# Performance work log

Hardware: AMD Instinct MI355X
Metric: run time of the kernel (lower is better)

## Reference

```python
import jax, jax.numpy as jnp
import numpy as np
from jax import lax

N_NODES = 16384
N_EDGES = 262144
T = 64
F_IN = 8
H1, C1 = 12, 16          # globals H and O in the source
HID2 = H1 * C1           # 192, input to second GATConv
LSTM_H = 128
TRAIN_LEN = 32
TARGET_ID = 0
NEG_SLOPE = 0.2


def setup_inputs() -> dict:
    key = jax.random.key(0)
    ks = jax.random.split(key, 16)
    x = jax.random.normal(ks[0], (T, N_NODES, F_IN), jnp.float32)
    src = jax.random.randint(ks[1], (T, N_EDGES), 0, N_NODES)
    dst = jax.random.randint(ks[2], (T, N_EDGES), 0, N_NODES)
    dst = jnp.where(dst == src, (dst + 1) % N_NODES, dst)  # guarantee no self-loops
    edge_index = jnp.stack([src, dst], axis=1)  # (T, 2, E)
    g = lambda k, sh: jax.random.normal(k, sh, jnp.float32) * 0.1
    return {
        "x": x, "edge_index": edge_index,
        "Wl1": g(ks[3], (F_IN, H1 * C1)),
        "att_l1": g(ks[4], (1, H1, C1)), "att_r1": g(ks[5], (1, H1, C1)),
        "b1": jnp.zeros((H1 * C1,), jnp.float32),
        "Wl2": g(ks[6], (HID2, 1)),
        "att_l2": g(ks[7], (1, 1, 1)), "att_r2": g(ks[8], (1, 1, 1)),
        "b2": jnp.zeros((1,), jnp.float32),
        "Wih0": g(ks[9], (4 * LSTM_H, 1)), "Whh0": g(ks[10], (4 * LSTM_H, LSTM_H)),
        "bih0": jnp.zeros((4 * LSTM_H,), jnp.float32), "bhh0": jnp.zeros((4 * LSTM_H,), jnp.float32),
        "Wih1": g(ks[11], (4 * LSTM_H, LSTM_H)), "Whh1": g(ks[12], (4 * LSTM_H, LSTM_H)),
        "bih1": jnp.zeros((4 * LSTM_H,), jnp.float32), "bhh1": jnp.zeros((4 * LSTM_H,), jnp.float32),
        "Wlin": g(ks[13], (1, LSTM_H)), "blin": jnp.zeros((1,), jnp.float32),
    }


def _gat(x, ei, W, att_l, att_r, b, heads, outc, concat):
    N = x.shape[0]
    xl = (x @ W).reshape(N, heads, outc)              # (N,H,C)
    al = jnp.sum(xl * att_l, axis=-1)                 # (N,H)
    ar = jnp.sum(xl * att_r, axis=-1)                 # (N,H)
    loop = jnp.arange(N)
    src = jnp.concatenate([ei[0], loop])              # add self loops (inputs have none)
    dst = jnp.concatenate([ei[1], loop])
    alpha = jax.nn.leaky_relu(al[src] + ar[dst], NEG_SLOPE)  # (E+N, H)
    # segment softmax over destination neighborhoods
    amax = jax.ops.segment_max(alpha, dst, num_segments=N)
    ex = jnp.exp(alpha - amax[dst])
    alpha = ex / (jax.ops.segment_sum(ex, dst, num_segments=N)[dst] + 1e-16)
    # hardcoded per-edge-row edits from message(): s and v copies, then blend
    s = alpha.at[jnp.array([1, 2, 12, 19, 22])].set(0.0).at[jnp.array([7, 14])].set(1.0)
    v = alpha.at[jnp.array([10, 13])].set(0.5).at[jnp.array([17])].set(0.0)
    alpha = 0.8 * alpha + 0.1 * s + 0.1 * v
    out = jax.ops.segment_sum(xl[src] * alpha[:, :, None], dst, num_segments=N)  # (N,H,C)
    out = out.reshape(N, heads * outc) if concat else out.mean(axis=1)
    return out + b


def _lstm_layer(xs, Wih, Whh, bih, bhh):
    # xs: (L, B, in) -> hs: (L, B, H); torch gate order i,f,g,o
    Bsz, Hd = xs.shape[1], Whh.shape[1]
    def step(carry, xt):
        h, c = carry
        gates = xt @ Wih.T + h @ Whh.T + bih + bhh
        i, f, g, o = jnp.split(gates, 4, axis=-1)
        c = jax.nn.sigmoid(f) * c + jax.nn.sigmoid(i) * jnp.tanh(g)
        h = jax.nn.sigmoid(o) * jnp.tanh(c)
        return (h, c), h
    init = (jnp.zeros((Bsz, Hd), xs.dtype), jnp.zeros((Bsz, Hd), xs.dtype))
    _, hs = lax.scan(step, init, xs)
    return hs


def reference(x, edge_index, Wl1, att_l1, att_r1, b1, Wl2, att_l2, att_r2, b2,
              Wih0, Whh0, bih0, bhh0, Wih1, Whh1, bih1, bhh1, Wlin, blin):
    def per_t(args):
        xt, eit = args
        h = _gat(xt, eit, Wl1, att_l1, att_r1, b1, H1, C1, True)
        h = jax.nn.elu(h)
        h = _gat(h, eit, Wl2, att_l2, att_r2, b2, 1, 1, False)
        return h[:, 0]
    out = lax.map(per_t, (x, edge_index))             # (T, N) == xs_out
    series = lax.stop_gradient(out[:, TARGET_ID])     # split_sequences detaches
    idx = jnp.arange(T - TRAIN_LEN)[:, None] + jnp.arange(TRAIN_LEN)[None, :]
    ts = series[idx][:, :, None]                      # (B, L, 1), batch_first
    xs = jnp.transpose(ts, (1, 0, 2))                 # (L, B, 1)
    hs = _lstm_layer(xs, Wih0, Whh0, bih0, bhh0)
    hs = _lstm_layer(hs, Wih1, Whh1, bih1, bhh1)
    return hs[-1] @ Wlin.T + blin                     # (B, 1)
```

## Files before the change

kernel.cpp:

```cpp
#include <hip/hip_runtime.h>
#include <math.h>

#define T 64
#define NN 16384
#define NE 262144
#define FIN 8
#define H1H 12
#define C1C 16
#define HID 192
#define CAP2 95
#define SCAP 96
#define DEGCAP 127
#define LH 128
#define G4 512
#define NB 32
#define NL 32

#define DEV __device__ __forceinline__

DEV float wave_max(float v){
  #pragma unroll
  for (int m = 32; m; m >>= 1) v = fmaxf(v, __shfl_xor(v, m));
  return v;
}
DEV float wave_sum(float v){
  #pragma unroll
  for (int m = 32; m; m >>= 1) v += __shfl_xor(v, m);
  return v;
}
DEV float leaky(float x){ return x >= 0.f ? x : 0.2f * x; }
DEV float sigmoidf(float x){ return 1.f / (1.f + expf(-x)); }

DEV float apply_edit(float a, int eid){
  if (eid >= 32) return a;
  const unsigned m09 = (1u<<1)|(1u<<2)|(1u<<7)|(1u<<10)|(1u<<12)|(1u<<13)|(1u<<14)|(1u<<17)|(1u<<19)|(1u<<22);
  const unsigned mp1 = (1u<<7)|(1u<<14);
  const unsigned mp05 = (1u<<10)|(1u<<13);
  unsigned b = 1u << eid;
  float r = (m09 & b) ? 0.9f * a : a;
  if (mp1 & b) r += 0.1f;
  if (mp05 & b) r += 0.05f;
  return r;
}

__global__ __launch_bounds__(256) void k_scan0(const int* __restrict__ ei,
                                               int* __restrict__ cnt2, int* __restrict__ list2){
  long long gid = (long long)blockIdx.x * blockDim.x + threadIdx.x;
  long long e4 = gid * 4;
  int t = (int)(e4 >> 18);
  int e = (int)(e4 & (NE - 1));
  const int* dstp = ei + (size_t)t * 2 * NE + NE + e;
  int4 d = *(const int4*)dstp;
  int dd[4] = {d.x, d.y, d.z, d.w};
  #pragma unroll
  for (int q = 0; q < 4; q++){
    if (dd[q] == 0){
      int pos = atomicAdd(&cnt2[t], 1);
      if (pos < CAP2) list2[t * CAP2 + pos] = e + q;
    }
  }
}

__global__ __launch_bounds__(128) void k_build(const int* __restrict__ ei, const int* __restrict__ cnt2,
                                               const int* __restrict__ list2, int* __restrict__ scnt,
                                               int* __restrict__ Slist, int* __restrict__ slot_of){
  int t = blockIdx.x;
  int* so = slot_of + (size_t)t * NN;
  int m = min(cnt2[t], CAP2);
  for (int i = threadIdx.x; i < m + 1; i += blockDim.x){
    int u = (i == m) ? 0 : ei[(size_t)t * 2 * NE + list2[t * CAP2 + i]];
    int old = atomicCAS(&so[u], -1, -2);
    if (old == -1){
      int s = atomicAdd(&scnt[t], 1);
      Slist[t * SCAP + s] = u;
      __hip_atomic_store(&so[u], s, __ATOMIC_RELAXED, __HIP_MEMORY_SCOPE_AGENT);
    }
  }
}

__global__ __launch_bounds__(256) void k_scan1(const int* __restrict__ ei, const int* __restrict__ slot_of,
                                               int* __restrict__ ecnt1, int* __restrict__ elist1){
  long long gid = (long long)blockIdx.x * blockDim.x + threadIdx.x;
  long long e4 = gid * 4;
  int t = (int)(e4 >> 18);
  int e = (int)(e4 & (NE - 1));
  const int* dstp = ei + (size_t)t * 2 * NE + NE + e;
  int4 d = *(const int4*)dstp;
  int dd[4] = {d.x, d.y, d.z, d.w};
  #pragma unroll
  for (int q = 0; q < 4; q++){
    int sl = slot_of[(size_t)t * NN + dd[q]];
    if (sl >= 0){
      int pos = atomicAdd(&ecnt1[t * SCAP + sl], 1);
      if (pos < DEGCAP) elist1[((size_t)t * SCAP + sl) * DEGCAP + pos] = e + q;
    }
  }
}

__global__ __launch_bounds__(64, 4) void k_gat1(const float* __restrict__ x, const int* __restrict__ ei,
                                             const float* __restrict__ Wl1, const float* __restrict__ attl,
                                             const float* __restrict__ attr, const float* __restrict__ b1,
                                             const int* __restrict__ scnt, const int* __restrict__ Slist,
                                             const int* __restrict__ ecnt1, const int* __restrict__ elist1,
                                             float* __restrict__ h1){
  int t = blockIdx.y, s = blockIdx.x, h = blockIdx.z;
  if (s >= scnt[t]) return;
  int lane = threadIdx.x;
  int u = Slist[t * SCAP + s];
  int deg = min(ecnt1[t * SCAP + s], DEGCAP);
  int tot = deg + 1;
  bool two = tot > 64;
  const float* xt = x + (size_t)t * NN * FIN;
  const int* srcp = ei + (size_t)t * 2 * NE;
  const int* el = elist1 + ((size_t)t * SCAP + s) * DEGCAP;

  float4 xu_a = ((const float4*)(xt + (size_t)u * FIN))[0];
  float4 xu_b = ((const float4*)(xt + (size_t)u * FIN))[1];
  float xu[FIN] = {xu_a.x, xu_a.y, xu_a.z, xu_a.w, xu_b.x, xu_b.y, xu_b.z, xu_b.w};

  bool act0 = lane < tot;
  int eid0 = 1 << 29;
  int su0 = u;
  if (lane < deg){ int e = el[lane]; eid0 = e; su0 = srcp[e]; }
  float4 xs0a = ((const float4*)(xt + (size_t)su0 * FIN))[0];
  float4 xs0b = ((const float4*)(xt + (size_t)su0 * FIN))[1];
  float xsrc0[FIN] = {xs0a.x, xs0a.y, xs0a.z, xs0a.w, xs0b.x, xs0b.y, xs0b.z, xs0b.w};

  bool act1 = false; int eid1 = 1 << 29;
  float xsrc1[FIN];
  if (two){
    int idx = 64 + lane;
    act1 = idx < tot;
    int su1 = u;
    if (idx < deg){ int e = el[idx]; eid1 = e; su1 = srcp[e]; }
    float4 xs1a = ((const float4*)(xt + (size_t)su1 * FIN))[0];
    float4 xs1b = ((const float4*)(xt + (size_t)su1 * FIN))[1];
    #pragma unroll
    for (int f = 0; f < 4; f++) xsrc1[f] = (&xs1a.x)[f];
    #pragma unroll
    for (int f = 0; f < 4; f++) xsrc1[4 + f] = (&xs1b.x)[f];
  }

  const float* Wh = Wl1 + h * C1C;
  const float* attlh = attl + h * C1C;
  const float* attrh = attr + h * C1C;

  float ar = 0.f;
  #pragma unroll
  for (int c = 0; c < C1C; c++){
    float v = 0.f;
    #pragma unroll
    for (int f = 0; f < FIN; f++) v = fmaf(xu[f], Wh[f * HID + c], v);
    ar = fmaf(v, attrh[c], ar);
  }

  float xls0[C1C];
  float al0 = 0.f;
  #pragma unroll
  for (int c = 0; c < C1C; c++){
    float v = 0.f;
    #pragma unroll
    for (int f = 0; f < FIN; f++) v = fmaf(xsrc0[f], Wh[f * HID + c], v);
    xls0[c] = v;
    al0 = fmaf(v, attlh[c], al0);
  }
  float raw0 = act0 ? leaky(al0 + ar) : -INFINITY;

  float xls1[C1C];
  float raw1 = -INFINITY;
  if (two){
    float al1 = 0.f;
    #pragma unroll
    for (int c = 0; c < C1C; c++){
      float v = 0.f;
      #pragma unroll
      for (int f = 0; f < FIN; f++) v = fmaf(xsrc1[f], Wh[f * HID + c], v);
      xls1[c] = v;
      al1 = fmaf(v, attlh[c], al1);
    }
    raw1 = act1 ? leaky(al1 + ar) : -INFINITY;
  }

  float M = wave_max(fmaxf(raw0, raw1));
  float ex0 = act0 ? expf(raw0 - M) : 0.f;
  float ex1 = act1 ? expf(raw1 - M) : 0.f;
  float S = wave_sum(ex0 + ex1);
  float den = S + 1e-16f;
  float alpha0 = apply_edit(ex0 / den, eid0);
  float alpha1 = two ? apply_edit(ex1 / den, eid1) : 0.f;

  float sum[C1C];
  #pragma unroll
  for (int c = 0; c < C1C; c++){
    sum[c] = xls0[c] * alpha0;
    if (two) sum[c] = fmaf(xls1[c], alpha1, sum[c]);
  }
  #pragma unroll
  for (int m = 32; m; m >>= 1){
    #pragma unroll
    for (int c = 0; c < C1C; c++) sum[c] += __shfl_xor(sum[c], m);
  }
  if (lane == 0){
    float* h1p = h1 + ((size_t)t * SCAP + s) * HID + h * C1C;
    #pragma unroll
    for (int c = 0; c < C1C; c++){
      float v = sum[c] + b1[h * C1C + c];
      h1p[c] = v > 0.f ? v : expm1f(v);
    }
  }
}

__global__ __launch_bounds__(64) void k_gat2(const int* __restrict__ ei, const float* __restrict__ Wl2,
                                             const float* __restrict__ attl2_, const float* __restrict__ attr2_,
                                             const float* __restrict__ b2, const int* __restrict__ cnt2,
                                             const int* __restrict__ list2, const int* __restrict__ slot_of,
                                             const float* __restrict__ h1, float* __restrict__ series){
  int t = blockIdx.x; int lane = threadIdx.x;
  int deg = min(cnt2[t], CAP2);
  int tot = deg + 1;
  const int* srcp = ei + (size_t)t * 2 * NE;
  const int* so = slot_of + (size_t)t * NN;
  float attl2 = attl2_[0], attr2 = attr2_[0];
  int sl0 = so[0];
  const float* h1t = h1 + (size_t)t * SCAP * HID;

  float x0 = 0.f;
  for (int k = 0; k < HID; k++) x0 += h1t[(size_t)sl0 * HID + k] * Wl2[k];

  bool act[2]; int eid[2]; float xl2[2];
  #pragma unroll
  for (int ch = 0; ch < 2; ch++){
    int idx = ch * 64 + lane;
    act[ch] = idx < tot;
    eid[ch] = 1 << 29;
    int sl = sl0;
    if (idx < deg){ int e = list2[t * CAP2 + idx]; eid[ch] = e; sl = so[srcp[e]]; }
    float v = 0.f;
    if (act[ch]) for (int k = 0; k < HID; k++) v += h1t[(size_t)sl * HID + k] * Wl2[k];
    xl2[ch] = v;
  }
  float raw[2];
  #pragma unroll
  for (int ch = 0; ch < 2; ch++) raw[ch] = act[ch] ? leaky(attl2 * xl2[ch] + attr2 * x0) : -INFINITY;
  float M = wave_max(fmaxf(raw[0], raw[1]));
  float ex[2];
  #pragma unroll
  for (int ch = 0; ch < 2; ch++) ex[ch] = act[ch] ? expf(raw[ch] - M) : 0.f;
  float S = wave_sum(ex[0] + ex[1]);
  float den = S + 1e-16f;
  float contrib = apply_edit(ex[0] / den, eid[0]) * xl2[0] + apply_edit(ex[1] / den, eid[1]) * xl2[1];
  contrib = wave_sum(contrib);
  if (lane == 0) series[t] = contrib + b2[0];
}

#define AT_LOADR(p)    __hip_atomic_load((p), __ATOMIC_RELAXED, __HIP_MEMORY_SCOPE_AGENT)
#define AT_STORER(p,v) __hip_atomic_store((p), (v), __ATOMIC_RELAXED, __HIP_MEMORY_SCOPE_AGENT)

#define REP32(M) M(0)M(1)M(2)M(3)M(4)M(5)M(6)M(7)M(8)M(9)M(10)M(11)M(12)M(13)M(14)M(15)\
                 M(16)M(17)M(18)M(19)M(20)M(21)M(22)M(23)M(24)M(25)M(26)M(27)M(28)M(29)M(30)M(31)
#define WDECL(i) float4 w##i;
#define WLOAD(i) w##i = Wr[i];
#define WPIN(i)  asm volatile("" : "+v"(w##i.x), "+v"(w##i.y), "+v"(w##i.z), "+v"(w##i.w));
#define WFMA(i)  { float4 hv = h4[i]; a0 = fmaf(w##i.x, hv.x, a0); a1 = fmaf(w##i.y, hv.y, a1); \
                   a2 = fmaf(w##i.z, hv.z, a2); a3 = fmaf(w##i.w, hv.w, a3); }

__global__ __launch_bounds__(512, 2) void k_lstm(const float* __restrict__ series,
    const float* __restrict__ Wih0, const float* __restrict__ Whh0,
    const float* __restrict__ bih0, const float* __restrict__ bhh0,
    const float* __restrict__ Wih1, const float* __restrict__ Whh1,
    const float* __restrict__ bih1, const float* __restrict__ bhh1,
    const float* __restrict__ Wlin, const float* __restrict__ blin,
    float* __restrict__ h0g, float* __restrict__ xpart,
    int* __restrict__ flagA, int* __restrict__ flagB, float* __restrict__ out){
  int j = threadIdx.x;
  int st = blockIdx.x >> 5;
  int b = blockIdx.x & 31;
  __shared__ __align__(16) float h_lds[LH];
  __shared__ __align__(16) float c_lds[LH];
  __shared__ float gate_lds[G4];
  __shared__ float s_series[NL];
  __shared__ int rdy_lds;
  const float4* h4 = (const float4*)h_lds;

  if (st == 0){
    const float4* Wr = (const float4*)(Whh0 + (size_t)j * LH);
    REP32(WDECL)
    REP32(WLOAD)
    REP32(WPIN)
    float wih = Wih0[j];
    float bsum = bih0[j] + bhh0[j];
    if (j < LH){ h_lds[j] = 0.f; c_lds[j] = 0.f; }
    if (j < NL) s_series[j] = series[b + j];
    __syncthreads();
    for (int t = 0; t < NL; t++){
      float a0 = 0.f, a1 = 0.f, a2 = 0.f, a3 = 0.f;
      REP32(WFMA)
      float acc = fmaf(wih, s_series[t], bsum) + (a0 + a1) + (a2 + a3);
      gate_lds[j] = acc;
      __syncthreads();
      if (j < LH){
        float ig = sigmoidf(gate_lds[j]);
        float fg = sigmoidf(gate_lds[LH + j]);
        float gg = tanhf(gate_lds[2 * LH + j]);
        float og = sigmoidf(gate_lds[3 * LH + j]);
        float c = fg * c_lds[j] + ig * gg;
        float h = og * tanhf(c);
        c_lds[j] = c; h_lds[j] = h;
        AT_STORER(&h0g[(b * NL + t) * LH + j], h);
      }
      __syncthreads();
      if (j == 0) AT_STORER(&flagA[b], t + 1);
    }
  } else if (st == 1){
    const float4* Wr = (const float4*)(Wih1 + (size_t)j * LH);
    REP32(WDECL)
    REP32(WLOAD)
    REP32(WPIN)
    int ready = 0;
    for (int t = 0; t < NL; t++){
      if (ready <= t){
        if (j == 0){
          int f;
          while ((f = AT_LOADR(&flagA[b])) < t + 1) __builtin_amdgcn_s_sleep(1);
          rdy_lds = f;
        }
        __syncthreads();
        ready = rdy_lds;
      }
      if (j < LH) h_lds[j] = AT_LOADR(&h0g[(b * NL + t) * LH + j]);
      __syncthreads();
      float a0 = 0.f, a1 = 0.f, a2 = 0.f, a3 = 0.f;
      REP32(WFMA)
      AT_STORER(&xpart[(b * NL + t) * G4 + j], (a0 + a1) + (a2 + a3));
      __syncthreads();
      if (j == 0) AT_STORER(&flagB[b], t + 1);
    }
  } else {
    const float4* Wr = (const float4*)(Whh1 + (size_t)j * LH);
    REP32(WDECL)
    REP32(WLOAD)
    REP32(WPIN)
    float bsum = bih1[j] + bhh1[j];
    if (j < LH){ h_lds[j] = 0.f; c_lds[j] = 0.f; }
    __syncthreads();
    int ready = 0;
    for (int t = 0; t < NL; t++){
      if (ready <= t){
        if (j == 0){
          int f;
          while ((f = AT_LOADR(&flagB[b])) < t + 1) __builtin_amdgcn_s_sleep(1);
          rdy_lds = f;
        }
        __syncthreads();
        ready = rdy_lds;
      }
      float xj = AT_LOADR(&xpart[(b * NL + t) * G4 + j]);
      float a0 = 0.f, a1 = 0.f, a2 = 0.f, a3 = 0.f;
      REP32(WFMA)
      float acc = xj + bsum + (a0 + a1) + (a2 + a3);
      gate_lds[j] = acc;
      __syncthreads();
      if (j < LH){
        float ig = sigmoidf(gate_lds[j]);
        float fg = sigmoidf(gate_lds[LH + j]);
        float gg = tanhf(gate_lds[2 * LH + j]);
        float og = sigmoidf(gate_lds[3 * LH + j]);
        float c = fg * c_lds[j] + ig * gg;
        float h = og * tanhf(c);
        c_lds[j] = c; h_lds[j] = h;
      }
      __syncthreads();
    }
    if (j == 0){
      float s2 = blin[0];
      for (int k = 0; k < LH; k++) s2 += Wlin[k] * h_lds[k];
      out[b] = s2;
    }
  }
}

extern "C" void kernel_launch(void* const* d_in, const int* in_sizes, int n_in,
                              void* d_out, int out_size, void* d_ws, size_t ws_size,
                              hipStream_t stream) {
  const float* x     = (const float*)d_in[0];
  const int*   ei    = (const int*)  d_in[1];
  const float* Wl1   = (const float*)d_in[2];
  const float* attl1 = (const float*)d_in[3];
  const float* attr1 = (const float*)d_in[4];
  const float* b1    = (const float*)d_in[5];
  const float* Wl2   = (const float*)d_in[6];
  const float* attl2 = (const float*)d_in[7];
  const float* attr2 = (const float*)d_in[8];
  const float* b2    = (const float*)d_in[9];
  const float* Wih0  = (const float*)d_in[10];
  const float* Whh0  = (const float*)d_in[11];
  const float* bih0  = (const float*)d_in[12];
  const float* bhh0  = (const float*)d_in[13];
  const float* Wih1  = (const float*)d_in[14];
  const float* Whh1  = (const float*)d_in[15];
  const float* bih1  = (const float*)d_in[16];
  const float* bhh1  = (const float*)d_in[17];
  const float* Wlin  = (const float*)d_in[18];
  const float* blin  = (const float*)d_in[19];
  float* out = (float*)d_out;

  char* wsb = (char*)d_ws;
  size_t off = 0;
  auto alloc = [&](size_t bytes)->void*{
    void* p = wsb + off;
    off += (bytes + 255) & ~(size_t)255;
    return p;
  };
  int* cnt2  = (int*)alloc(T * 4);
  int* scnt  = (int*)alloc(T * 4);
  int* ecnt1 = (int*)alloc(T * SCAP * 4);
  int* flagA = (int*)alloc(NB * 4);
  int* flagB = (int*)alloc(NB * 4);
  size_t ctrl_bytes = off;
  int* slot_of = (int*)alloc((size_t)T * NN * 4);
  int* list2   = (int*)alloc((size_t)T * CAP2 * 4);
  int* Slist   = (int*)alloc((size_t)T * SCAP * 4);
  int* elist1  = (int*)alloc((size_t)T * SCAP * DEGCAP * 4);
  float* h1    = (float*)alloc((size_t)T * SCAP * HID * 4);
  float* series= (float*)alloc(T * 4);
  float* h0g   = (float*)alloc((size_t)NB * NL * LH * 4);
  float* xpart = (float*)alloc((size_t)NB * NL * G4 * 4);

  hipMemsetAsync(d_ws, 0, ctrl_bytes, stream);
  hipMemsetAsync(slot_of, 0xFF, (size_t)T * NN * 4, stream);

  k_scan0<<<T * NE / 4 / 256, 256, 0, stream>>>(ei, cnt2, list2);
  k_build<<<T, 128, 0, stream>>>(ei, cnt2, list2, scnt, Slist, slot_of);
  k_scan1<<<T * NE / 4 / 256, 256, 0, stream>>>(ei, slot_of, ecnt1, elist1);
  k_gat1<<<dim3(SCAP, T, H1H), 64, 0, stream>>>(x, ei, Wl1, attl1, attr1, b1, scnt, Slist, ecnt1, elist1, h1);
  k_gat2<<<T, 64, 0, stream>>>(ei, Wl2, attl2, attr2, b2, cnt2, list2, slot_of, h1, series);
  k_lstm<<<96, 512, 0, stream>>>(series, Wih0, Whh0, bih0, bhh0, Wih1, Whh1, bih1, bhh1,
                                 Wlin, blin, h0g, xpart, flagA, flagB, out);
}
```

Measured before the change: 415.7 us.

## Compact GAT1 work list and split LSTM weights between registers and LDS

k_build now appends each (t, slot) pair to a global work list. k_gat1 runs as a persistent grid-stride kernel over that list times the heads, instead of a sparse 3D grid where most blocks exit early. In the LSTM kernel only half of each weight row stays pinned in registers and the other half is staged transposed in LDS, which cuts register pressure at the cost of LDS reads every step. The LSTM consumer waits now poll the flag every step instead of caching a readiness counter.

```diff
diff --git a/kernel.cpp b/kernel.cpp
--- a/kernel.cpp
+++ b/kernel.cpp
@@ -63,7 +63,8 @@
 
 __global__ __launch_bounds__(128) void k_build(const int* __restrict__ ei, const int* __restrict__ cnt2,
                                                const int* __restrict__ list2, int* __restrict__ scnt,
-                                               int* __restrict__ Slist, int* __restrict__ slot_of){
+                                               int* __restrict__ Slist, int* __restrict__ slot_of,
+                                               int* __restrict__ wcnt, int* __restrict__ wlist){
   int t = blockIdx.x;
   int* so = slot_of + (size_t)t * NN;
   int m = min(cnt2[t], CAP2);
@@ -73,6 +74,8 @@
     if (old == -1){
       int s = atomicAdd(&scnt[t], 1);
       Slist[t * SCAP + s] = u;
+      int w = atomicAdd(wcnt, 1);
+      wlist[w] = (t << 8) | s;
       __hip_atomic_store(&so[u], s, __ATOMIC_RELAXED, __HIP_MEMORY_SCOPE_AGENT);
     }
   }
@@ -97,115 +100,125 @@
   }
 }
 
-__global__ __launch_bounds__(64, 4) void k_gat1(const float* __restrict__ x, const int* __restrict__ ei,
+__global__ __launch_bounds__(256, 4) void k_gat1(const float* __restrict__ x, const int* __restrict__ ei,
                                              const float* __restrict__ Wl1, const float* __restrict__ attl,
                                              const float* __restrict__ attr, const float* __restrict__ b1,
-                                             const int* __restrict__ scnt, const int* __restrict__ Slist,
+                                             const int* __restrict__ wcnt, const int* __restrict__ wlist,
+                                             const int* __restrict__ Slist,
                                              const int* __restrict__ ecnt1, const int* __restrict__ elist1,
                                              float* __restrict__ h1){
-  int t = blockIdx.y, s = blockIdx.x, h = blockIdx.z;
-  if (s >= scnt[t]) return;
-  int lane = threadIdx.x;
-  int u = Slist[t * SCAP + s];
-  int deg = min(ecnt1[t * SCAP + s], DEGCAP);
-  int tot = deg + 1;
-  bool two = tot > 64;
-  const float* xt = x + (size_t)t * NN * FIN;
-  const int* srcp = ei + (size_t)t * 2 * NE;
-  const int* el = elist1 + ((size_t)t * SCAP + s) * DEGCAP;
-
-  float4 xu_a = ((const float4*)(xt + (size_t)u * FIN))[0];
-  float4 xu_b = ((const float4*)(xt + (size_t)u * FIN))[1];
-  float xu[FIN] = {xu_a.x, xu_a.y, xu_a.z, xu_a.w, xu_b.x, xu_b.y, xu_b.z, xu_b.w};
-
-  bool act0 = lane < tot;
-  int eid0 = 1 << 29;
-  int su0 = u;
-  if (lane < deg){ int e = el[lane]; eid0 = e; su0 = srcp[e]; }
-  float4 xs0a = ((const float4*)(xt + (size_t)su0 * FIN))[0];
-  float4 xs0b = ((const float4*)(xt + (size_t)su0 * FIN))[1];
-  float xsrc0[FIN] = {xs0a.x, xs0a.y, xs0a.z, xs0a.w, xs0b.x, xs0b.y, xs0b.z, xs0b.w};
-
-  bool act1 = false; int eid1 = 1 << 29;
-  float xsrc1[FIN];
-  if (two){
-    int idx = 64 + lane;
-    act1 = idx < tot;
-    int su1 = u;
-    if (idx < deg){ int e = el[idx]; eid1 = e; su1 = srcp[e]; }
-    float4 xs1a = ((const float4*)(xt + (size_t)su1 * FIN))[0];
-    float4 xs1b = ((const float4*)(xt + (size_t)su1 * FIN))[1];
-    #pragma unroll
-    for (int f = 0; f < 4; f++) xsrc1[f] = (&xs1a.x)[f];
-    #pragma unroll
-    for (int f = 0; f < 4; f++) xsrc1[4 + f] = (&xs1b.x)[f];
-  }
-
-  const float* Wh = Wl1 + h * C1C;
-  const float* attlh = attl + h * C1C;
-  const float* attrh = attr + h * C1C;
-
-  float ar = 0.f;
-  #pragma unroll
-  for (int c = 0; c < C1C; c++){
-    float v = 0.f;
-    #pragma unroll
-    for (int f = 0; f < FIN; f++) v = fmaf(xu[f], Wh[f * HID + c], v);
-    ar = fmaf(v, attrh[c], ar);
-  }
-
-  float xls0[C1C];
-  float al0 = 0.f;
-  #pragma unroll
-  for (int c = 0; c < C1C; c++){
-    float v = 0.f;
-    #pragma unroll
-    for (int f = 0; f < FIN; f++) v = fmaf(xsrc0[f], Wh[f * HID + c], v);
-    xls0[c] = v;
-    al0 = fmaf(v, attlh[c], al0);
-  }
-  float raw0 = act0 ? leaky(al0 + ar) : -INFINITY;
-
-  float xls1[C1C];
-  float raw1 = -INFINITY;
-  if (two){
-    float al1 = 0.f;
+  int lane = threadIdx.x & 63;
+  int wid = blockIdx.x * (blockDim.x >> 6) + (threadIdx.x >> 6);
+  int nwaves = gridDim.x * (blockDim.x >> 6);
+  int ntask = wcnt[0] * H1H;
+
+  for (int task = wid; task < ntask; task += nwaves){
+    int pi = task / H1H;
+    int h = task - pi * H1H;
+    int pair = wlist[pi];
+    int t = pair >> 8, s = pair & 255;
+
+    int u = Slist[t * SCAP + s];
+    int deg = min(ecnt1[t * SCAP + s], DEGCAP);
+    int tot = deg + 1;
+    bool two = tot > 64;
+    const float* xt = x + (size_t)t * NN * FIN;
+    const int* srcp = ei + (size_t)t * 2 * NE;
+    const int* el = elist1 + ((size_t)t * SCAP + s) * DEGCAP;
+
+    float4 xu_a = ((const float4*)(xt + (size_t)u * FIN))[0];
+    float4 xu_b = ((const float4*)(xt + (size_t)u * FIN))[1];
+    float xu[FIN] = {xu_a.x, xu_a.y, xu_a.z, xu_a.w, xu_b.x, xu_b.y, xu_b.z, xu_b.w};
+
+    bool act0 = lane < tot;
+    int eid0 = 1 << 29;
+    int su0 = u;
+    if (lane < deg){ int e = el[lane]; eid0 = e; su0 = srcp[e]; }
+    float4 xs0a = ((const float4*)(xt + (size_t)su0 * FIN))[0];
+    float4 xs0b = ((const float4*)(xt + (size_t)su0 * FIN))[1];
+    float xsrc0[FIN] = {xs0a.x, xs0a.y, xs0a.z, xs0a.w, xs0b.x, xs0b.y, xs0b.z, xs0b.w};
+
+    bool act1 = false; int eid1 = 1 << 29;
+    float xsrc1[FIN];
+    if (two){
+      int idx = 64 + lane;
+      act1 = idx < tot;
+      int su1 = u;
+      if (idx < deg){ int e = el[idx]; eid1 = e; su1 = srcp[e]; }
+      float4 xs1a = ((const float4*)(xt + (size_t)su1 * FIN))[0];
+      float4 xs1b = ((const float4*)(xt + (size_t)su1 * FIN))[1];
+      #pragma unroll
+      for (int f = 0; f < 4; f++) xsrc1[f] = (&xs1a.x)[f];
+      #pragma unroll
+      for (int f = 0; f < 4; f++) xsrc1[4 + f] = (&xs1b.x)[f];
+    }
+
+    const float* Wh = Wl1 + h * C1C;
+    const float* attlh = attl + h * C1C;
+    const float* attrh = attr + h * C1C;
+
+    float ar = 0.f;
     #pragma unroll
     for (int c = 0; c < C1C; c++){
       float v = 0.f;
       #pragma unroll
-      for (int f = 0; f < FIN; f++) v = fmaf(xsrc1[f], Wh[f * HID + c], v);
-      xls1[c] = v;
-      al1 = fmaf(v, attlh[c], al1);
-    }
-    raw1 = act1 ? leaky(al1 + ar) : -INFINITY;
-  }
-
-  float M = wave_max(fmaxf(raw0, raw1));
-  float ex0 = act0 ? expf(raw0 - M) : 0.f;
-  float ex1 = act1 ? expf(raw1 - M) : 0.f;
-  float S = wave_sum(ex0 + ex1);
-  float den = S + 1e-16f;
-  float alpha0 = apply_edit(ex0 / den, eid0);
-  float alpha1 = two ? apply_edit(ex1 / den, eid1) : 0.f;
-
-  float sum[C1C];
-  #pragma unroll
-  for (int c = 0; c < C1C; c++){
-    sum[c] = xls0[c] * alpha0;
-    if (two) sum[c] = fmaf(xls1[c], alpha1, sum[c]);
-  }
-  #pragma unroll
-  for (int m = 32; m; m >>= 1){
-    #pragma unroll
-    for (int c = 0; c < C1C; c++) sum[c] += __shfl_xor(sum[c], m);
-  }
-  if (lane == 0){
-    float* h1p = h1 + ((size_t)t * SCAP + s) * HID + h * C1C;
+      for (int f = 0; f < FIN; f++) v = fmaf(xu[f], Wh[f * HID + c], v);
+      ar = fmaf(v, attrh[c], ar);
+    }
+
+    float xls0[C1C];
+    float al0 = 0.f;
     #pragma unroll
     for (int c = 0; c < C1C; c++){
-      float v = sum[c] + b1[h * C1C + c];
-      h1p[c] = v > 0.f ? v : expm1f(v);
+      float v = 0.f;
+      #pragma unroll
+      for (int f = 0; f < FIN; f++) v = fmaf(xsrc0[f], Wh[f * HID + c], v);
+      xls0[c] = v;
+      al0 = fmaf(v, attlh[c], al0);
+    }
+    float raw0 = act0 ? leaky(al0 + ar) : -INFINITY;
+
+    float xls1[C1C];
+    float raw1 = -INFINITY;
+    if (two){
+      float al1 = 0.f;
+      #pragma unroll
+      for (int c = 0; c < C1C; c++){
+        float v = 0.f;
+        #pragma unroll
+        for (int f = 0; f < FIN; f++) v = fmaf(xsrc1[f], Wh[f * HID + c], v);
+        xls1[c] = v;
+        al1 = fmaf(v, attlh[c], al1);
+      }
+      raw1 = act1 ? leaky(al1 + ar) : -INFINITY;
+    }
+
+    float M = wave_max(fmaxf(raw0, raw1));
+    float ex0 = act0 ? expf(raw0 - M) : 0.f;
+    float ex1 = act1 ? expf(raw1 - M) : 0.f;
+    float S = wave_sum(ex0 + ex1);
+    float den = S + 1e-16f;
+    float alpha0 = apply_edit(ex0 / den, eid0);
+    float alpha1 = two ? apply_edit(ex1 / den, eid1) : 0.f;
+
+    float sum[C1C];
+    #pragma unroll
+    for (int c = 0; c < C1C; c++){
+      sum[c] = xls0[c] * alpha0;
+      if (two) sum[c] = fmaf(xls1[c], alpha1, sum[c]);
+    }
+    #pragma unroll
+    for (int m = 32; m; m >>= 1){
+      #pragma unroll
+      for (int c = 0; c < C1C; c++) sum[c] += __shfl_xor(sum[c], m);
+    }
+    if (lane == 0){
+      float* h1p = h1 + ((size_t)t * SCAP + s) * HID + h * C1C;
+      #pragma unroll
+      for (int c = 0; c < C1C; c++){
+        float v = sum[c] + b1[h * C1C + c];
+        h1p[c] = v > 0.f ? v : expm1f(v);
+      }
     }
   }
 }
@@ -256,12 +269,11 @@
 #define AT_LOADR(p)    __hip_atomic_load((p), __ATOMIC_RELAXED, __HIP_MEMORY_SCOPE_AGENT)
 #define AT_STORER(p,v) __hip_atomic_store((p), (v), __ATOMIC_RELAXED, __HIP_MEMORY_SCOPE_AGENT)
 
-#define REP32(M) M(0)M(1)M(2)M(3)M(4)M(5)M(6)M(7)M(8)M(9)M(10)M(11)M(12)M(13)M(14)M(15)\
-                 M(16)M(17)M(18)M(19)M(20)M(21)M(22)M(23)M(24)M(25)M(26)M(27)M(28)M(29)M(30)M(31)
+#define REP16(M) M(0)M(1)M(2)M(3)M(4)M(5)M(6)M(7)M(8)M(9)M(10)M(11)M(12)M(13)M(14)M(15)
 #define WDECL(i) float4 w##i;
 #define WLOAD(i) w##i = Wr[i];
 #define WPIN(i)  asm volatile("" : "+v"(w##i.x), "+v"(w##i.y), "+v"(w##i.z), "+v"(w##i.w));
-#define WFMA(i)  { float4 hv = h4[i]; a0 = fmaf(w##i.x, hv.x, a0); a1 = fmaf(w##i.y, hv.y, a1); \
+#define WFMA(i)  { float4 hv = h4b[i]; a0 = fmaf(w##i.x, hv.x, a0); a1 = fmaf(w##i.y, hv.y, a1); \
                    a2 = fmaf(w##i.z, hv.z, a2); a3 = fmaf(w##i.w, hv.w, a3); }
 
 __global__ __launch_bounds__(512, 2) void k_lstm(const float* __restrict__ series,
@@ -275,18 +287,22 @@
   int j = threadIdx.x;
   int st = blockIdx.x >> 5;
   int b = blockIdx.x & 31;
+  __shared__ float4 Wt4[16 * 512];
   __shared__ __align__(16) float h_lds[LH];
-  __shared__ __align__(16) float c_lds[LH];
+  __shared__ float c_lds[LH];
   __shared__ float gate_lds[G4];
   __shared__ float s_series[NL];
-  __shared__ int rdy_lds;
-  const float4* h4 = (const float4*)h_lds;
+  const float4* h4b = (const float4*)h_lds;
+
+  const float* Wsrc = (st == 0) ? Whh0 : (st == 1) ? Wih1 : Whh1;
+  const float4* Wr = (const float4*)(Wsrc + (size_t)j * LH);
+  REP16(WDECL)
+  REP16(WLOAD)
+  REP16(WPIN)
+  #pragma unroll
+  for (int q = 0; q < 16; q++) Wt4[q * 512 + j] = Wr[16 + q];
 
   if (st == 0){
-    const float4* Wr = (const float4*)(Whh0 + (size_t)j * LH);
-    REP32(WDECL)
-    REP32(WLOAD)
-    REP32(WPIN)
     float wih = Wih0[j];
     float bsum = bih0[j] + bhh0[j];
     if (j < LH){ h_lds[j] = 0.f; c_lds[j] = 0.f; }
@@ -294,9 +310,15 @@
     __syncthreads();
     for (int t = 0; t < NL; t++){
       float a0 = 0.f, a1 = 0.f, a2 = 0.f, a3 = 0.f;
-      REP32(WFMA)
-      float acc = fmaf(wih, s_series[t], bsum) + (a0 + a1) + (a2 + a3);
-      gate_lds[j] = acc;
+      REP16(WFMA)
+      #pragma unroll
+      for (int q = 0; q < 16; q++){
+        float4 hv = h4b[16 + q];
+        float4 wv = Wt4[q * 512 + j];
+        a0 = fmaf(wv.x, hv.x, a0); a1 = fmaf(wv.y, hv.y, a1);
+        a2 = fmaf(wv.z, hv.z, a2); a3 = fmaf(wv.w, hv.w, a3);
+      }
+      gate_lds[j] = fmaf(wih, s_series[t], bsum) + (a0 + a1) + (a2 + a3);
       __syncthreads();
       if (j < LH){
         float ig = sigmoidf(gate_lds[j]);
@@ -312,53 +334,47 @@
       if (j == 0) AT_STORER(&flagA[b], t + 1);
     }
   } else if (st == 1){
-    const float4* Wr = (const float4*)(Wih1 + (size_t)j * LH);
-    REP32(WDECL)
-    REP32(WLOAD)
-    REP32(WPIN)
-    int ready = 0;
+    __syncthreads();
     for (int t = 0; t < NL; t++){
-      if (ready <= t){
-        if (j == 0){
-          int f;
-          while ((f = AT_LOADR(&flagA[b])) < t + 1) __builtin_amdgcn_s_sleep(1);
-          rdy_lds = f;
-        }
-        __syncthreads();
-        ready = rdy_lds;
-      }
+      if (j == 0){
+        while (AT_LOADR(&flagA[b]) < t + 1) __builtin_amdgcn_s_sleep(1);
+      }
+      __syncthreads();
       if (j < LH) h_lds[j] = AT_LOADR(&h0g[(b * NL + t) * LH + j]);
       __syncthreads();
       float a0 = 0.f, a1 = 0.f, a2 = 0.f, a3 = 0.f;
-      REP32(WFMA)
+      REP16(WFMA)
+      #pragma unroll
+      for (int q = 0; q < 16; q++){
+        float4 hv = h4b[16 + q];
+        float4 wv = Wt4[q * 512 + j];
+        a0 = fmaf(wv.x, hv.x, a0); a1 = fmaf(wv.y, hv.y, a1);
+        a2 = fmaf(wv.z, hv.z, a2); a3 = fmaf(wv.w, hv.w, a3);
+      }
       AT_STORER(&xpart[(b * NL + t) * G4 + j], (a0 + a1) + (a2 + a3));
       __syncthreads();
       if (j == 0) AT_STORER(&flagB[b], t + 1);
     }
   } else {
-    const float4* Wr = (const float4*)(Whh1 + (size_t)j * LH);
-    REP32(WDECL)
-    REP32(WLOAD)
-    REP32(WPIN)
     float bsum = bih1[j] + bhh1[j];
     if (j < LH){ h_lds[j] = 0.f; c_lds[j] = 0.f; }
     __syncthreads();
-    int ready = 0;
     for (int t = 0; t < NL; t++){
-      if (ready <= t){
-        if (j == 0){
-          int f;
-          while ((f = AT_LOADR(&flagB[b])) < t + 1) __builtin_amdgcn_s_sleep(1);
-          rdy_lds = f;
-        }
-        __syncthreads();
-        ready = rdy_lds;
-      }
+      if (j == 0){
+        while (AT_LOADR(&flagB[b]) < t + 1) __builtin_amdgcn_s_sleep(1);
+      }
+      __syncthreads();
       float xj = AT_LOADR(&xpart[(b * NL + t) * G4 + j]);
       float a0 = 0.f, a1 = 0.f, a2 = 0.f, a3 = 0.f;
-      REP32(WFMA)
-      float acc = xj + bsum + (a0 + a1) + (a2 + a3);
-      gate_lds[j] = acc;
+      REP16(WFMA)
+      #pragma unroll
+      for (int q = 0; q < 16; q++){
+        float4 hv = h4b[16 + q];
+        float4 wv = Wt4[q * 512 + j];
+        a0 = fmaf(wv.x, hv.x, a0); a1 = fmaf(wv.y, hv.y, a1);
+        a2 = fmaf(wv.z, hv.z, a2); a3 = fmaf(wv.w, hv.w, a3);
+      }
+      gate_lds[j] = xj + bsum + (a0 + a1) + (a2 + a3);
       __syncthreads();
       if (j < LH){
         float ig = sigmoidf(gate_lds[j]);
@@ -416,10 +432,12 @@
   int* ecnt1 = (int*)alloc(T * SCAP * 4);
   int* flagA = (int*)alloc(NB * 4);
   int* flagB = (int*)alloc(NB * 4);
+  int* wcnt  = (int*)alloc(4);
   size_t ctrl_bytes = off;
   int* slot_of = (int*)alloc((size_t)T * NN * 4);
   int* list2   = (int*)alloc((size_t)T * CAP2 * 4);
   int* Slist   = (int*)alloc((size_t)T * SCAP * 4);
+  int* wlist   = (int*)alloc((size_t)T * SCAP * 4);
   int* elist1  = (int*)alloc((size_t)T * SCAP * DEGCAP * 4);
   float* h1    = (float*)alloc((size_t)T * SCAP * HID * 4);
   float* series= (float*)alloc(T * 4);
@@ -430,9 +448,9 @@
   hipMemsetAsync(slot_of, 0xFF, (size_t)T * NN * 4, stream);
 
   k_scan0<<<T * NE / 4 / 256, 256, 0, stream>>>(ei, cnt2, list2);
-  k_build<<<T, 128, 0, stream>>>(ei, cnt2, list2, scnt, Slist, slot_of);
+  k_build<<<T, 128, 0, stream>>>(ei, cnt2, list2, scnt, Slist, slot_of, wcnt, wlist);
   k_scan1<<<T * NE / 4 / 256, 256, 0, stream>>>(ei, slot_of, ecnt1, elist1);
-  k_gat1<<<dim3(SCAP, T, H1H), 64, 0, stream>>>(x, ei, Wl1, attl1, attr1, b1, scnt, Slist, ecnt1, elist1, h1);
+  k_gat1<<<512, 256, 0, stream>>>(x, ei, Wl1, attl1, attr1, b1, wcnt, wlist, Slist, ecnt1, elist1, h1);
   k_gat2<<<T, 64, 0, stream>>>(ei, Wl2, attl2, attr2, b2, cnt2, list2, slot_of, h1, series);
   k_lstm<<<96, 512, 0, stream>>>(series, Wih0, Whh0, bih0, bhh0, Wih1, Whh1, bih1, bhh1,
                                  Wlin, blin, h0g, xpart, flagA, flagB, out);
```

New measurement: 495.2 us. +19.1%, slower.
